# Kernel optimization log

Hardware: AMD Instinct MI355X
Metric: run time of the kernel (lower is better)

## Reference

```python
import jax, jax.numpy as jnp
import numpy as np

BETA = 0.25

def setup_inputs() -> dict:
    key = jax.random.key(0)
    k1, k2 = jax.random.split(key)
    x = jax.random.normal(k1, (32, 32, 32, 64), dtype=jnp.float32)
    # tf.random_uniform_initializer default: uniform in [-0.05, 0.05]
    embeddings = jax.random.uniform(k2, (64, 1024), dtype=jnp.float32,
                                    minval=-0.05, maxval=0.05)
    return {"x": x, "embeddings": embeddings}

def reference(x, embeddings):
    D, K = embeddings.shape
    flat = x.reshape(-1, D)                                   # [N, D]
    # squared L2 distances to each codebook vector (expanded form)
    sim = flat @ embeddings                                   # [N, K]
    dists = (jnp.sum(flat * flat, axis=1, keepdims=True)
             + jnp.sum(embeddings * embeddings, axis=0)
             - 2.0 * sim)                                     # [N, K]
    idx = jnp.argmin(dists, axis=1)                           # [N]
    quantized = embeddings.T[idx].reshape(x.shape)            # gather == one-hot matmul
    commitment_loss = BETA * jnp.mean((jax.lax.stop_gradient(quantized) - x) ** 2)
    codebook_loss = jnp.mean((quantized - jax.lax.stop_gradient(x)) ** 2)
    loss = commitment_loss + codebook_loss
    out = x + jax.lax.stop_gradient(quantized - x)            # straight-through
    return out, loss
```

## Files before the change

### kernel.cpp

```cpp
#include <hip/hip_runtime.h>
#include <hip/hip_bf16.h>


#define NROWS 32768
#define DDIM  64
#define KCODE 1024
#define NELEM (NROWS * DDIM)
#define MARGIN 2.5e-4f
#define FIXBLOCKS 256

typedef __attribute__((ext_vector_type(8))) short bf16x8;
typedef __attribute__((ext_vector_type(4))) float f32x4;

static __device__ __forceinline__ unsigned short f2bf(float v) {
    __hip_bfloat16 h = __float2bfloat16(v);
    unsigned short b;
    __builtin_memcpy(&b, &h, 2);
    return b;
}
static __device__ __forceinline__ float bf2f(unsigned short b) {
    unsigned int u = ((unsigned int)b) << 16;
    float f;
    __builtin_memcpy(&f, &u, 4);
    return f;
}

__global__ void vq_prep(const float* __restrict__ e,
                        float* __restrict__ se,
                        float* __restrict__ eT,
                        unsigned short* __restrict__ ehT,
                        unsigned short* __restrict__ elT,
                        int* __restrict__ ctrl) {
    __shared__ float tile[64][17];
    const int t = threadIdx.x;
    const int k0 = blockIdx.x * 16;
    if (blockIdx.x == 0 && t < 4) ctrl[t] = 0;
    #pragma unroll
    for (int i = 0; i < 4; ++i) {
        int idx = i * 256 + t;
        int d = idx >> 4, kk = idx & 15;
        tile[d][kk] = e[d * KCODE + k0 + kk];
    }
    __syncthreads();
    if (t < 16) {
        float s = 0.f;
        #pragma unroll
        for (int d = 0; d < 64; ++d) { float v = tile[d][t]; s = fmaf(v, v, s); }
        se[k0 + t] = s;
    }
    const int kk = t >> 4;
    const int dg = (t & 15) * 4;
    float v0 = tile[dg + 0][kk], v1 = tile[dg + 1][kk];
    float v2 = tile[dg + 2][kk], v3 = tile[dg + 3][kk];
    *(float4*)&eT[(size_t)(k0 + kk) * 64 + dg] = make_float4(v0, v1, v2, v3);
    unsigned short h0 = f2bf(v0), h1 = f2bf(v1), h2 = f2bf(v2), h3 = f2bf(v3);
    *(ushort4*)&ehT[(size_t)(k0 + kk) * 64 + dg] = make_ushort4(h0, h1, h2, h3);
    *(ushort4*)&elT[(size_t)(k0 + kk) * 64 + dg] =
        make_ushort4(f2bf(v0 - bf2f(h0)), f2bf(v1 - bf2f(h1)),
                     f2bf(v2 - bf2f(h2)), f2bf(v3 - bf2f(h3)));
}

__attribute__((amdgpu_waves_per_eu(2, 2)))
__launch_bounds__(256)
__global__ void vq_main(const float* __restrict__ x,
                        const float* __restrict__ se,
                        const float* __restrict__ eT,
                        const unsigned short* __restrict__ ehT,
                        const unsigned short* __restrict__ elT,
                        float* __restrict__ out,
                        float* __restrict__ lossAcc,
                        int* __restrict__ cnt,
                        int2* __restrict__ list) {
    __shared__ float Lb [64][65];
    __shared__ float Lb2[64][65];
    __shared__ int   Li [64][65];
    __shared__ int   rowIdx[64];
    __shared__ float wsum[4];

    const int t = threadIdx.x;
    const int lane = t & 63;
    const int w = t >> 6;
    const int quad = lane >> 4, l15 = lane & 15;
    const int rowBlk = blockIdx.x * 64;

    bf16x8 ah[4][2], al[4][2];
    #pragma unroll
    for (int mt = 0; mt < 4; ++mt) {
        #pragma unroll
        for (int ks = 0; ks < 2; ++ks) {
            const float4* ap = (const float4*)(x + (size_t)(rowBlk + mt * 16 + l15) * 64
                                               + ks * 32 + quad * 8);
            float4 a0 = ap[0], a1 = ap[1];
            float av[8] = {a0.x, a0.y, a0.z, a0.w, a1.x, a1.y, a1.z, a1.w};
            bf16x8 h, l;
            #pragma unroll
            for (int j = 0; j < 8; ++j) {
                unsigned short hb = f2bf(av[j]);
                h[j] = (short)hb;
                l[j] = (short)f2bf(av[j] - bf2f(hb));
            }
            ah[mt][ks] = h; al[mt][ks] = l;
        }
    }

    float sb[4][4], sb2[4][4];
    int   si[4][4];
    #pragma unroll
    for (int mt = 0; mt < 4; ++mt)
        #pragma unroll
        for (int r = 0; r < 4; ++r) { sb[mt][r] = 3.4e38f; sb2[mt][r] = 3.4e38f; si[mt][r] = 0; }

    const int cbase = w * 256;
    const size_t bStr = (size_t)64;
    bf16x8 h0[4], h1[4], l0[4], l1[4];
    float sen[4];
    #pragma unroll
    for (int p = 0; p < 4; ++p) {
        const int nl = cbase + p * 16 + l15;
        const bf16x8* hp = (const bf16x8*)(ehT + (size_t)nl * bStr + quad * 8);
        const bf16x8* lp = (const bf16x8*)(elT + (size_t)nl * bStr + quad * 8);
        h0[p] = hp[0]; h1[p] = hp[4]; l0[p] = lp[0]; l1[p] = lp[4];
        sen[p] = se[nl];
    }

    #pragma unroll 4
    for (int nt = 0; nt < 16; ++nt) {
        const int p = nt & 3;
        bf16x8 ch0 = h0[p], ch1 = h1[p], cl0 = l0[p], cl1 = l1[p];
        float cse = sen[p];
        {
            const int nl = cbase + (nt + 4) * 16 + l15;
            const bf16x8* hp = (const bf16x8*)(ehT + (size_t)nl * bStr + quad * 8);
            const bf16x8* lp = (const bf16x8*)(elT + (size_t)nl * bStr + quad * 8);
            h0[p] = hp[0]; h1[p] = hp[4]; l0[p] = lp[0]; l1[p] = lp[4];
            sen[p] = se[nl];
        }
        const int nl = cbase + nt * 16 + l15;
        #pragma unroll
        for (int mt = 0; mt < 4; ++mt) {
            f32x4 aA = {0.f, 0.f, 0.f, 0.f}, aB = {0.f, 0.f, 0.f, 0.f};
            aA = __builtin_amdgcn_mfma_f32_16x16x32_bf16(ah[mt][0], ch0, aA, 0, 0, 0);
            aB = __builtin_amdgcn_mfma_f32_16x16x32_bf16(ah[mt][1], ch1, aB, 0, 0, 0);
            aA = __builtin_amdgcn_mfma_f32_16x16x32_bf16(ah[mt][0], cl0, aA, 0, 0, 0);
            aB = __builtin_amdgcn_mfma_f32_16x16x32_bf16(ah[mt][1], cl1, aB, 0, 0, 0);
            aA = __builtin_amdgcn_mfma_f32_16x16x32_bf16(al[mt][0], ch0, aA, 0, 0, 0);
            aB = __builtin_amdgcn_mfma_f32_16x16x32_bf16(al[mt][1], ch1, aB, 0, 0, 0);
            #pragma unroll
            for (int r = 0; r < 4; ++r) {
                float key = fmaf(-2.f, aA[r] + aB[r], cse);
                bool lt = key < sb[mt][r];
                sb2[mt][r] = fminf(sb2[mt][r], fmaxf(sb[mt][r], key));
                sb[mt][r]  = fminf(sb[mt][r], key);
                si[mt][r]  = lt ? nl : si[mt][r];
            }
        }
    }

    const int col = w * 16 + l15;
    #pragma unroll
    for (int mt = 0; mt < 4; ++mt)
        #pragma unroll
        for (int r = 0; r < 4; ++r) {
            int rr = mt * 16 + quad * 4 + r;
            Lb [rr][col] = sb [mt][r];
            Lb2[rr][col] = sb2[mt][r];
            Li [rr][col] = si [mt][r];
        }
    __syncthreads();

    if (t < 64) {
        float B = Lb[t][0], B2 = Lb2[t][0];
        int I = Li[t][0];
        for (int c = 1; c < 64; ++c) {
            float b = Lb[t][c], b2 = Lb2[t][c];
            int i = Li[t][c];
            float nB2 = fminf(fminf(B2, b2), fmaxf(B, b));
            bool take = (b < B) || (b == B && i < I);
            B = take ? b : B;
            I = take ? i : I;
            B2 = nB2;
        }
        rowIdx[t] = I;
        if (B2 - B < MARGIN) {
            int p = atomicAdd(cnt, 1);
            list[p] = make_int2(rowBlk + t, I);
        }
    }
    __syncthreads();

    {
        const int rl = w * 16 + l15;
        const int idx = rowIdx[rl];
        const float4* qrow = (const float4*)(eT + (size_t)idx * 64 + quad * 16);
        const float4* xrow = (const float4*)(x + (size_t)(rowBlk + rl) * 64 + quad * 16);
        float4* orow = (float4*)(out + (size_t)(rowBlk + rl) * 64 + quad * 16);
        float lsum = 0.f;
        #pragma unroll
        for (int i = 0; i < 4; ++i) {
            float4 q = qrow[i];
            float4 xv = xrow[i];
            float4 o;
            float dx;
            dx = q.x - xv.x; o.x = xv.x + dx; lsum = fmaf(dx, dx, lsum);
            dx = q.y - xv.y; o.y = xv.y + dx; lsum = fmaf(dx, dx, lsum);
            dx = q.z - xv.z; o.z = xv.z + dx; lsum = fmaf(dx, dx, lsum);
            dx = q.w - xv.w; o.w = xv.w + dx; lsum = fmaf(dx, dx, lsum);
            orow[i] = o;
        }
        #pragma unroll
        for (int off = 32; off > 0; off >>= 1)
            lsum += __shfl_down(lsum, off, 64);
        if (lane == 0) wsum[w] = lsum;
    }
    __syncthreads();
    if (t == 0)
        atomicAdd(lossAcc, wsum[0] + wsum[1] + wsum[2] + wsum[3]);
}

__launch_bounds__(256)
__global__ void vq_fix(const float* __restrict__ x,
                       const float* __restrict__ se,
                       const float* __restrict__ eT,
                       const int2* __restrict__ list,
                       const int* __restrict__ cnt,
                       float* __restrict__ lossAcc,
                       int* __restrict__ done,
                       float* __restrict__ out) {
    __shared__ float xs[64];
    __shared__ float cb[256];
    __shared__ int   ci[256];
    __shared__ int   newIdxS;
    const int t = threadIdx.x;
    const int n = *cnt;

    for (int i = blockIdx.x; i < n; i += gridDim.x) {
        int2 en = list[i];
        const int row = en.x, oldIdx = en.y;
        if (t < 64) xs[t] = x[(size_t)row * 64 + t];
        __syncthreads();

        float sx = 0.f;
        #pragma unroll
        for (int d = 0; d < 64; ++d) sx = fmaf(xs[d], xs[d], sx);

        const int k0 = t * 4;
        const float4* e0 = (const float4*)(eT + (size_t)(k0 + 0) * 64);
        const float4* e1 = (const float4*)(eT + (size_t)(k0 + 1) * 64);
        const float4* e2 = (const float4*)(eT + (size_t)(k0 + 2) * 64);
        const float4* e3 = (const float4*)(eT + (size_t)(k0 + 3) * 64);
        float dot0 = 0.f, dot1 = 0.f, dot2 = 0.f, dot3 = 0.f;
        #pragma unroll
        for (int i4 = 0; i4 < 16; ++i4) {
            float4 v0 = e0[i4], v1 = e1[i4], v2 = e2[i4], v3 = e3[i4];
            float xa = xs[4 * i4 + 0], xb = xs[4 * i4 + 1];
            float xc = xs[4 * i4 + 2], xd = xs[4 * i4 + 3];
            dot0 = fmaf(xa, v0.x, dot0); dot0 = fmaf(xb, v0.y, dot0);
            dot0 = fmaf(xc, v0.z, dot0); dot0 = fmaf(xd, v0.w, dot0);
            dot1 = fmaf(xa, v1.x, dot1); dot1 = fmaf(xb, v1.y, dot1);
            dot1 = fmaf(xc, v1.z, dot1); dot1 = fmaf(xd, v1.w, dot1);
            dot2 = fmaf(xa, v2.x, dot2); dot2 = fmaf(xb, v2.y, dot2);
            dot2 = fmaf(xc, v2.z, dot2); dot2 = fmaf(xd, v2.w, dot2);
            dot3 = fmaf(xa, v3.x, dot3); dot3 = fmaf(xb, v3.y, dot3);
            dot3 = fmaf(xc, v3.z, dot3); dot3 = fmaf(xd, v3.w, dot3);
        }
        float dd0 = (sx + se[k0 + 0]) - 2.0f * dot0;
        float dd1 = (sx + se[k0 + 1]) - 2.0f * dot1;
        float dd2 = (sx + se[k0 + 2]) - 2.0f * dot2;
        float dd3 = (sx + se[k0 + 3]) - 2.0f * dot3;
        float db = dd0; int di = k0;
        if (dd1 < db) { db = dd1; di = k0 + 1; }
        if (dd2 < db) { db = dd2; di = k0 + 2; }
        if (dd3 < db) { db = dd3; di = k0 + 3; }
        cb[t] = db; ci[t] = di;
        __syncthreads();

        if (t < 64) {
            float B = cb[t]; int I = ci[t];
            #pragma unroll
            for (int s = 64; s < 256; s += 64) {
                float b = cb[t + s]; int i2 = ci[t + s];
                bool take = (b < B) || (b == B && i2 < I);
                B = take ? b : B;
                I = take ? i2 : I;
            }
            #pragma unroll
            for (int m = 1; m < 64; m <<= 1) {
                float ob = __shfl_xor(B, m, 64);
                int   oi = __shfl_xor(I, m, 64);
                bool take = (ob < B) || (ob == B && oi < I);
                B = take ? ob : B;
                I = take ? oi : I;
            }
            if (t == 0) newIdxS = I;
        }
        __syncthreads();

        const int ni = newIdxS;
        if (ni != oldIdx) {
            if (t < 64) {
                float xv = xs[t];
                float qn = eT[(size_t)ni * 64 + t];
                float qo = eT[(size_t)oldIdx * 64 + t];
                float dn = qn - xv, dl = qo - xv;
                out[(size_t)row * 64 + t] = xv + dn;
                float delta = dn * dn - dl * dl;
                #pragma unroll
                for (int off = 32; off > 0; off >>= 1)
                    delta += __shfl_down(delta, off, 64);
                if (t == 0) atomicAdd(lossAcc, delta);
            }
        }
        __syncthreads();
    }

    if (t == 0) {
        __threadfence();
        int fin = atomicAdd(done, 1);
        if (fin == FIXBLOCKS - 1) {
            float s = atomicAdd(lossAcc, 0.0f);
            float m = s / (float)NELEM;
            out[NELEM] = 0.25f * m + m;
        }
    }
}

extern "C" void kernel_launch(void* const* d_in, const int* in_sizes, int n_in,
                              void* d_out, int out_size, void* d_ws, size_t ws_size,
                              hipStream_t stream) {
    const float* x = (const float*)d_in[0];
    const float* e = (const float*)d_in[1];
    float* out = (float*)d_out;
    float* ws  = (float*)d_ws;

    float* lossAcc      = ws;
    int*   cnt          = (int*)(ws + 1);
    int*   done         = (int*)(ws + 2);
    float* se           = ws + 64;
    float* eT           = ws + 1280;
    unsigned short* ehT = (unsigned short*)(ws + 66816);
    unsigned short* elT = (unsigned short*)(ws + 101632);
    int2*  list         = (int2*)(ws + 136448);

    vq_prep<<<64, 256, 0, stream>>>(e, se, eT, ehT, elT, (int*)ws);
    vq_main<<<NROWS / 64, 256, 0, stream>>>(x, se, eT, ehT, elT, out, lossAcc, cnt, list);
    vq_fix<<<FIXBLOCKS, 256, 0, stream>>>(x, se, eT, list, cnt, lossAcc, done, out);
}
```

Baseline: 111.9 us.

## Halve rows per block, raise waves per EU, parallelize row reduction with shuffles

Result: slower. 123.2 us (+10.1%).

```diff
diff --git a/kernel.cpp b/kernel.cpp
--- a/kernel.cpp
+++ b/kernel.cpp
@@ -60,7 +60,7 @@
                      f2bf(v2 - bf2f(h2)), f2bf(v3 - bf2f(h3)));
 }
 
-__attribute__((amdgpu_waves_per_eu(2, 2)))
+__attribute__((amdgpu_waves_per_eu(4, 4)))
 __launch_bounds__(256)
 __global__ void vq_main(const float* __restrict__ x,
                         const float* __restrict__ se,
@@ -71,21 +71,21 @@
                         float* __restrict__ lossAcc,
                         int* __restrict__ cnt,
                         int2* __restrict__ list) {
-    __shared__ float Lb [64][65];
-    __shared__ float Lb2[64][65];
-    __shared__ int   Li [64][65];
-    __shared__ int   rowIdx[64];
+    __shared__ float Lb [32][65];
+    __shared__ float Lb2[32][65];
+    __shared__ int   Li [32][65];
+    __shared__ int   rowIdx[32];
     __shared__ float wsum[4];
 
     const int t = threadIdx.x;
     const int lane = t & 63;
     const int w = t >> 6;
     const int quad = lane >> 4, l15 = lane & 15;
-    const int rowBlk = blockIdx.x * 64;
-
-    bf16x8 ah[4][2], al[4][2];
-    #pragma unroll
-    for (int mt = 0; mt < 4; ++mt) {
+    const int rowBlk = blockIdx.x * 32;
+
+    bf16x8 ah[2][2], al[2][2];
+    #pragma unroll
+    for (int mt = 0; mt < 2; ++mt) {
         #pragma unroll
         for (int ks = 0; ks < 2; ++ks) {
             const float4* ap = (const float4*)(x + (size_t)(rowBlk + mt * 16 + l15) * 64
@@ -103,41 +103,40 @@
         }
     }
 
-    float sb[4][4], sb2[4][4];
-    int   si[4][4];
-    #pragma unroll
-    for (int mt = 0; mt < 4; ++mt)
+    float sb[2][4], sb2[2][4];
+    int   si[2][4];
+    #pragma unroll
+    for (int mt = 0; mt < 2; ++mt)
         #pragma unroll
         for (int r = 0; r < 4; ++r) { sb[mt][r] = 3.4e38f; sb2[mt][r] = 3.4e38f; si[mt][r] = 0; }
 
     const int cbase = w * 256;
-    const size_t bStr = (size_t)64;
-    bf16x8 h0[4], h1[4], l0[4], l1[4];
-    float sen[4];
-    #pragma unroll
-    for (int p = 0; p < 4; ++p) {
+    bf16x8 h0[2], h1[2], l0[2], l1[2];
+    float sen[2];
+    #pragma unroll
+    for (int p = 0; p < 2; ++p) {
         const int nl = cbase + p * 16 + l15;
-        const bf16x8* hp = (const bf16x8*)(ehT + (size_t)nl * bStr + quad * 8);
-        const bf16x8* lp = (const bf16x8*)(elT + (size_t)nl * bStr + quad * 8);
+        const bf16x8* hp = (const bf16x8*)(ehT + (size_t)nl * 64 + quad * 8);
+        const bf16x8* lp = (const bf16x8*)(elT + (size_t)nl * 64 + quad * 8);
         h0[p] = hp[0]; h1[p] = hp[4]; l0[p] = lp[0]; l1[p] = lp[4];
         sen[p] = se[nl];
     }
 
-    #pragma unroll 4
+    #pragma unroll 2
     for (int nt = 0; nt < 16; ++nt) {
-        const int p = nt & 3;
+        const int p = nt & 1;
         bf16x8 ch0 = h0[p], ch1 = h1[p], cl0 = l0[p], cl1 = l1[p];
         float cse = sen[p];
         {
-            const int nl = cbase + (nt + 4) * 16 + l15;
-            const bf16x8* hp = (const bf16x8*)(ehT + (size_t)nl * bStr + quad * 8);
-            const bf16x8* lp = (const bf16x8*)(elT + (size_t)nl * bStr + quad * 8);
+            const int nl = cbase + (nt + 2) * 16 + l15;
+            const bf16x8* hp = (const bf16x8*)(ehT + (size_t)nl * 64 + quad * 8);
+            const bf16x8* lp = (const bf16x8*)(elT + (size_t)nl * 64 + quad * 8);
             h0[p] = hp[0]; h1[p] = hp[4]; l0[p] = lp[0]; l1[p] = lp[4];
             sen[p] = se[nl];
         }
         const int nl = cbase + nt * 16 + l15;
         #pragma unroll
-        for (int mt = 0; mt < 4; ++mt) {
+        for (int mt = 0; mt < 2; ++mt) {
             f32x4 aA = {0.f, 0.f, 0.f, 0.f}, aB = {0.f, 0.f, 0.f, 0.f};
             aA = __builtin_amdgcn_mfma_f32_16x16x32_bf16(ah[mt][0], ch0, aA, 0, 0, 0);
             aB = __builtin_amdgcn_mfma_f32_16x16x32_bf16(ah[mt][1], ch1, aB, 0, 0, 0);
@@ -158,7 +157,7 @@
 
     const int col = w * 16 + l15;
     #pragma unroll
-    for (int mt = 0; mt < 4; ++mt)
+    for (int mt = 0; mt < 2; ++mt)
         #pragma unroll
         for (int r = 0; r < 4; ++r) {
             int rr = mt * 16 + quad * 4 + r;
@@ -168,35 +167,51 @@
         }
     __syncthreads();
 
-    if (t < 64) {
-        float B = Lb[t][0], B2 = Lb2[t][0];
-        int I = Li[t][0];
-        for (int c = 1; c < 64; ++c) {
-            float b = Lb[t][c], b2 = Lb2[t][c];
-            int i = Li[t][c];
+    {
+        const int r = t >> 3, seg = t & 7;
+        const int c0 = seg * 8;
+        float B = Lb[r][c0], B2 = Lb2[r][c0];
+        int   I = Li[r][c0];
+        #pragma unroll
+        for (int c = 1; c < 8; ++c) {
+            float b = Lb[r][c0 + c], b2 = Lb2[r][c0 + c];
+            int i = Li[r][c0 + c];
             float nB2 = fminf(fminf(B2, b2), fmaxf(B, b));
             bool take = (b < B) || (b == B && i < I);
             B = take ? b : B;
             I = take ? i : I;
             B2 = nB2;
         }
-        rowIdx[t] = I;
-        if (B2 - B < MARGIN) {
-            int p = atomicAdd(cnt, 1);
-            list[p] = make_int2(rowBlk + t, I);
+        #pragma unroll
+        for (int m = 1; m < 8; m <<= 1) {
+            float ob  = __shfl_xor(B,  m, 64);
+            float ob2 = __shfl_xor(B2, m, 64);
+            int   oi  = __shfl_xor(I,  m, 64);
+            float nB2 = fminf(fminf(B2, ob2), fmaxf(B, ob));
+            bool take = (ob < B) || (ob == B && oi < I);
+            B = take ? ob : B;
+            I = take ? oi : I;
+            B2 = nB2;
+        }
+        if (seg == 0) {
+            rowIdx[r] = I;
+            if (B2 - B < MARGIN) {
+                int p = atomicAdd(cnt, 1);
+                list[p] = make_int2(rowBlk + r, I);
+            }
         }
     }
     __syncthreads();
 
     {
-        const int rl = w * 16 + l15;
-        const int idx = rowIdx[rl];
-        const float4* qrow = (const float4*)(eT + (size_t)idx * 64 + quad * 16);
-        const float4* xrow = (const float4*)(x + (size_t)(rowBlk + rl) * 64 + quad * 16);
-        float4* orow = (float4*)(out + (size_t)(rowBlk + rl) * 64 + quad * 16);
+        const int r = t >> 3, c = (t & 7) * 8;
+        const int idx = rowIdx[r];
+        const float4* qrow = (const float4*)(eT + (size_t)idx * 64 + c);
+        const float4* xrow = (const float4*)(x + (size_t)(rowBlk + r) * 64 + c);
+        float4* orow = (float4*)(out + (size_t)(rowBlk + r) * 64 + c);
         float lsum = 0.f;
         #pragma unroll
-        for (int i = 0; i < 4; ++i) {
+        for (int i = 0; i < 2; ++i) {
             float4 q = qrow[i];
             float4 xv = xrow[i];
             float4 o;
@@ -342,6 +357,6 @@
     int2*  list         = (int2*)(ws + 136448);
 
     vq_prep<<<64, 256, 0, stream>>>(e, se, eT, ehT, elT, (int*)ws);
-    vq_main<<<NROWS / 64, 256, 0, stream>>>(x, se, eT, ehT, elT, out, lossAcc, cnt, list);
+    vq_main<<<NROWS / 32, 256, 0, stream>>>(x, se, eT, ehT, elT, out, lossAcc, cnt, list);
     vq_fix<<<FIXBLOCKS, 256, 0, stream>>>(x, se, eT, list, cnt, lossAcc, done, out);
 }
```
